# Optimization experiments

Measured on AMD Instinct MI355X. Metric: run time of the kernel, lower is better.

The kernel has to match this reference:

```python
import jax, jax.numpy as jnp
import numpy as np

D_MODEL = 640
KW = 32                                  # kernel_width -> content_kernel (compression (1,1))
SUPER = np.array([5, 5, 2, 1, 1])        # supersampling per subhead
DIL = np.array([1, 1, 2, 4, 8])          # dilation rate per subhead
SUBHEADS = 5
HEADS = int(SUPER.sum())                 # 14
DH = D_MODEL // SUBHEADS                 # 128
B, N = 2, 1024
KC = KW                                  # content kernel width
DIL_PER_HEAD = np.repeat(DIL, SUPER)     # dilation used by each of the 14 value heads


def _windows(seq, bias, dil):
    """Banded (dilated, stride-1, 'same'-padded) windows of a projected sequence.

    seq: (B, N, DH). The original zero-pads the raw sequence, then applies the
    per-head Linear; projecting a zero vector yields the bias, so padding the
    projected sequence with `bias` is mathematically identical.
    Returns (B, N, KC, DH) with out[b, l, j] = padded[b, l + j*dil].
    """
    dil = int(dil)
    pad_total = (KC - 1) * dil           # effective kernel minus 1, stride 1 -> same length
    pl = pad_total // 2
    pr = pad_total - pl
    b = seq.shape[0]
    left = jnp.broadcast_to(bias, (b, pl, DH))
    right = jnp.broadcast_to(bias, (b, pr, DH))
    padded = jnp.concatenate([left, seq, right], axis=1)
    idx = jnp.arange(N)[:, None] + jnp.arange(KC)[None, :] * dil  # (N, KC)
    return padded[:, idx]


def setup_inputs() -> dict:
    key = jax.random.key(0)
    ks = jax.random.split(key, 13)
    f = lambda k, sh, s=1.0: jax.random.normal(k, sh, dtype=jnp.float32) * s
    return {
        "query": f(ks[0], (B, N, D_MODEL)),
        "key": f(ks[1], (B, N, D_MODEL)),
        "value": f(ks[2], (B, N, D_MODEL)),
        "Qk": f(ks[3], (SUBHEADS, DH, D_MODEL), 0.04),
        "Qb": f(ks[4], (SUBHEADS, DH), 0.02),
        "Kk": f(ks[5], (SUBHEADS, DH, D_MODEL), 0.04),
        "Kb": f(ks[6], (SUBHEADS, DH), 0.02),
        "Vk": f(ks[7], (HEADS, DH, D_MODEL), 0.04),
        "Vb": f(ks[8], (HEADS, DH), 0.02),
        "Sk": f(ks[9], (HEADS, KC, KC), 0.1),   # Pos_Sampling kernel, Kq=1 so in=out=KC
        "Sb": f(ks[10], (HEADS, KC), 0.02),
        "Ck": f(ks[11], (D_MODEL, HEADS * DH), 0.02),  # Collapse kernel
        "Cb": f(ks[12], (D_MODEL,), 0.0),
    }


def reference(query, key, value, Qk, Qb, Kk, Kb, Vk, Vb, Sk, Sb, Ck, Cb):
    # Per-subhead Q/K projections (query_kernel=1, stride=1 -> one query per position)
    q = jnp.einsum('bnd,sod->bnso', query, Qk) + Qb          # (B,N,5,DH)
    kproj = jnp.einsum('bnd,sod->bnso', key, Kk) + Kb        # (B,N,5,DH)
    kwin = jnp.stack(
        [_windows(kproj[:, :, s], Kb[s], DIL[s]) for s in range(SUBHEADS)],
        axis=2)                                              # (B,N,5,KC,DH)
    # Banded scores (original applies no 1/sqrt(d) scaling)
    score = jnp.einsum('bnsd,bnskd->bnsk', q, kwin)          # (B,N,5,KC)
    # Supersample subhead scores into heads, then learned positional resampling
    score = jnp.repeat(score, SUPER, axis=2, total_repeat_length=HEADS)  # (B,N,14,KC)
    score = jnp.einsum('bnhk,hjk->bnhj', score, Sk) + Sb     # Pos_Sampling Linear
    w = jax.nn.softmax(score, axis=-1)
    # Per-head value projection; each head windows with its subhead's dilation
    vproj = jnp.einsum('bnd,hod->bnho', value, Vk) + Vb      # (B,N,14,DH)
    vwin = jnp.stack(
        [_windows(vproj[:, :, h], Vb[h], DIL_PER_HEAD[h]) for h in range(HEADS)],
        axis=2)                                              # (B,N,14,KC,DH)
    attn = jnp.einsum('bnhk,bnhkd->bnhd', w, vwin)           # (B,N,14,DH)
    flat = attn.reshape(attn.shape[0], attn.shape[1], HEADS * DH)
    return jnp.einsum('bnf,of->bno', flat, Ck) + Cb          # (B,N,D_MODEL)
```

## Files before the change

### kernel.cpp

```cpp
#include <hip/hip_runtime.h>
#include <hip/hip_bf16.h>

using bf16 = __hip_bfloat16;
typedef __attribute__((ext_vector_type(8))) short s16x8;
typedef __attribute__((ext_vector_type(4))) float f32x4;
typedef unsigned int u32;

__device__ __forceinline__ float b2f(short u) {
    union { float f; u32 i; } x; x.i = ((u32)(unsigned short)u) << 16; return x.f;
}
__device__ __forceinline__ short f2b(float f) {
    bf16 h = (bf16)f; return *(short*)&h;
}

struct CvtArgs { const float* src[10]; bf16* dst[10]; int n[10]; int bb[11]; };
__global__ __launch_bounds__(256)
void convert_kernel(CvtArgs a) {
    const int blk = blockIdx.x;
    int s = 0;
    while (s < 9 && blk >= a.bb[s + 1]) ++s;
    const int base = (blk - a.bb[s]) * 1024 + threadIdx.x * 4;
    if (base >= a.n[s]) return;
    float4 v = *(const float4*)(a.src[s] + base);
    ushort4 o;
    o.x = (unsigned short)f2b(v.x); o.y = (unsigned short)f2b(v.y);
    o.z = (unsigned short)f2b(v.z); o.w = (unsigned short)f2b(v.w);
    *(ushort4*)(a.dst[s] + base) = o;
}

template<int BM, int BN, bool A_F32, bool OUT_F32>
__device__ __forceinline__ void gemm_pipe(
    const void* __restrict__ A, const bf16* __restrict__ W,
    const bf16* __restrict__ bias, void* __restrict__ out,
    int m0, int n0, int N, int K, bf16* lA, bf16* lB) {
    constexpr int WM = BM / 2, WN = BN / 2, FM = WM / 16, FN = WN / 16;
    constexpr int SA = BM / 64, SB = BN / 64;
    const int tid = threadIdx.x;
    const int wave = tid >> 6, lane = tid & 63;
    const int wr = wave >> 1, wc = wave & 1;
    const int quad = lane >> 4, lm = lane & 15;
    uint4 ra[SA], rb[SB];

    auto loadA = [&](int k0) {
#pragma unroll
        for (int q = 0; q < SA; ++q) {
            const int sl = q * 256 + tid, row = sl >> 2, col = (sl & 3) * 8;
            if (A_F32) {
                const float* g = (const float*)A + (size_t)(m0 + row) * K + k0 + col;
                float4 f0 = *(const float4*)g;
                float4 f1 = *(const float4*)(g + 4);
                union { uint4 u; short h[8]; } p;
                p.h[0] = f2b(f0.x); p.h[1] = f2b(f0.y); p.h[2] = f2b(f0.z); p.h[3] = f2b(f0.w);
                p.h[4] = f2b(f1.x); p.h[5] = f2b(f1.y); p.h[6] = f2b(f1.z); p.h[7] = f2b(f1.w);
                ra[q] = p.u;
            } else {
                ra[q] = *(const uint4*)((const bf16*)A + (size_t)(m0 + row) * K + k0 + col);
            }
        }
    };
    auto loadB = [&](int k0) {
#pragma unroll
        for (int q = 0; q < SB; ++q) {
            const int sl = q * 256 + tid, row = sl >> 2, col = (sl & 3) * 8;
            rb[q] = *(const uint4*)(W + (size_t)(n0 + row) * K + k0 + col);
        }
    };

    f32x4 acc[FM][FN] = {};
    loadA(0); loadB(0);
    for (int k0 = 0; k0 < K; k0 += 32) {
#pragma unroll
        for (int q = 0; q < SA; ++q) *(uint4*)(lA + (q * 256 + tid) * 8) = ra[q];
#pragma unroll
        for (int q = 0; q < SB; ++q) *(uint4*)(lB + (q * 256 + tid) * 8) = rb[q];
        __syncthreads();
        if (k0 + 32 < K) { loadA(k0 + 32); loadB(k0 + 32); }
        s16x8 af[FM], bf_[FN];
#pragma unroll
        for (int i = 0; i < FM; ++i)
            af[i] = *(const s16x8*)&lA[(wr * WM + i * 16 + lm) * 32 + quad * 8];
#pragma unroll
        for (int j = 0; j < FN; ++j)
            bf_[j] = *(const s16x8*)&lB[(wc * WN + j * 16 + lm) * 32 + quad * 8];
#pragma unroll
        for (int i = 0; i < FM; ++i)
#pragma unroll
            for (int j = 0; j < FN; ++j)
                acc[i][j] = __builtin_amdgcn_mfma_f32_16x16x32_bf16(af[i], bf_[j], acc[i][j], 0, 0, 0);
        __syncthreads();
    }
#pragma unroll
    for (int i = 0; i < FM; ++i) {
        const int rbase = m0 + wr * WM + i * 16 + quad * 4;
#pragma unroll
        for (int j = 0; j < FN; ++j) {
            const int col = n0 + wc * WN + j * 16 + lm;
            const float bv = (float)bias[col];
#pragma unroll
            for (int r = 0; r < 4; ++r) {
                float v = acc[i][j][r] + bv;
                size_t off = (size_t)(rbase + r) * N + col;
                if (OUT_F32) ((float*)out)[off] = v;
                else         ((bf16*)out)[off] = (bf16)v;
            }
        }
    }
}

__global__ __launch_bounds__(256)
void proj_kernel(const float* __restrict__ q, const float* __restrict__ k,
                 const float* __restrict__ v,
                 const bf16* __restrict__ Qkc, const bf16* __restrict__ Kkc,
                 const bf16* __restrict__ Vkc,
                 const bf16* __restrict__ Qbc, const bf16* __restrict__ Kbc,
                 const bf16* __restrict__ Vbc,
                 float* __restrict__ qp, float* __restrict__ kp,
                 bf16* __restrict__ vp) {
    __shared__ __align__(16) bf16 lA[128 * 32];
    __shared__ __align__(16) bf16 lB[64 * 32];
    const int L = blockIdx.x, xcd = L & 7, i = L >> 3;
    const int m0 = (xcd * 2 + i / 48) * 128;
    const int nid = i % 48;
    if (nid < 10)
        gemm_pipe<128, 64, true, true >(q, Qkc, Qbc, qp, m0, nid * 64, 640, 640, lA, lB);
    else if (nid < 20)
        gemm_pipe<128, 64, true, true >(k, Kkc, Kbc, kp, m0, (nid - 10) * 64, 640, 640, lA, lB);
    else
        gemm_pipe<128, 64, true, false>(v, Vkc, Vbc, vp, m0, (nid - 20) * 64, 1792, 640, lA, lB);
}

__global__ __launch_bounds__(256)
void collapse_kernel(const bf16* __restrict__ atn, const bf16* __restrict__ Ckc,
                     const bf16* __restrict__ Cbc, float* __restrict__ out) {
    __shared__ __align__(16) bf16 lA[64 * 32];
    __shared__ __align__(16) bf16 lB[64 * 32];
    const int L = blockIdx.x, xcd = L & 7, i = L >> 3;
    const int m0 = (xcd * 4 + i / 10) * 64;
    const int n0 = (i % 10) * 64;
    gemm_pipe<64, 64, false, true>(atn, Ckc, Cbc, out, m0, n0, 640, 1792, lA, lB);
}

__global__ __launch_bounds__(256)
void attn_v4(const float* __restrict__ qp, const float* __restrict__ kp,
             const bf16* __restrict__ vp,
             const bf16* __restrict__ Kbc, const bf16* __restrict__ Vbc,
             const bf16* __restrict__ Skc, const bf16* __restrict__ Sbc,
             bf16* __restrict__ atn) {
    const int pos = ((blockIdx.x & 7) << 8) | (blockIdx.x >> 3);
    const int b = pos >> 10, l = pos & 1023;
    const int t = threadIdx.x;
    __shared__ float qs[640];
    __shared__ float sc5[5 * 32];
    __shared__ float sc14[14 * 32];
    __shared__ float w14T[32 * 14];

    if (t < 160) ((float4*)qs)[t] = ((const float4*)(qp + (size_t)pos * 640))[t];
    __syncthreads();

    {
        const int j = t >> 3, p = t & 7;
#pragma unroll
        for (int s = 0; s < 5; ++s) {
            const int dil = (s < 2) ? 1 : (1 << (s - 1));
            const int pl = (31 * dil) >> 1;
            const int row = l + j * dil - pl;
            const float* q = qs + s * 128 + p * 4;
            float acc = 0.f;
            if (row >= 0 && row < 1024) {
                const float* kr = kp + (size_t)((b << 10) | row) * 640 + s * 128 + p * 4;
#pragma unroll
                for (int g = 0; g < 4; ++g) {
                    float4 kv = *(const float4*)(kr + g * 32);
                    float4 qv = *(const float4*)(q + g * 32);
                    acc += qv.x * kv.x + qv.y * kv.y + qv.z * kv.z + qv.w * kv.w;
                }
            } else {
                const bf16* kb = Kbc + s * 128 + p * 4;
#pragma unroll
                for (int g = 0; g < 4; ++g) {
                    float4 qv = *(const float4*)(q + g * 32);
                    acc += qv.x * (float)kb[g * 32] + qv.y * (float)kb[g * 32 + 1]
                         + qv.z * (float)kb[g * 32 + 2] + qv.w * (float)kb[g * 32 + 3];
                }
            }
            acc += __shfl_xor(acc, 1);
            acc += __shfl_xor(acc, 2);
            acc += __shfl_xor(acc, 4);
            if (p == 0) sc5[s * 32 + j] = acc;
        }
    }
    __syncthreads();

    for (int idx = t; idx < 448; idx += 256) {
        const int h = idx >> 5;
        const int s = (h < 5) ? 0 : (h < 10) ? 1 : (h < 12) ? 2 : (h == 12) ? 3 : 4;
        const s16x8* sk = (const s16x8*)((const short*)Skc + idx * 32);
        const float* sc = sc5 + s * 32;
        float acc = b2f(((const short*)Sbc)[idx]);
#pragma unroll
        for (int g = 0; g < 4; ++g) {
            s16x8 kk = sk[g];
#pragma unroll
            for (int r = 0; r < 8; ++r) acc += sc[g * 8 + r] * b2f(kk[r]);
        }
        sc14[idx] = acc;
    }
    __syncthreads();

    if (t < 224) {
        const int h = t >> 4, u = t & 15;
        float s0 = sc14[h * 32 + u], s1 = sc14[h * 32 + u + 16];
        float mx = fmaxf(s0, s1);
#pragma unroll
        for (int m = 1; m < 16; m <<= 1) mx = fmaxf(mx, __shfl_xor(mx, m));
        float e0 = __expf(s0 - mx), e1 = __expf(s1 - mx);
        float sum = e0 + e1;
#pragma unroll
        for (int m = 1; m < 16; m <<= 1) sum += __shfl_xor(sum, m);
        float inv = 1.f / sum;
        w14T[u * 14 + h] = e0 * inv;
        w14T[(u + 16) * 14 + h] = e1 * inv;
    }
    __syncthreads();

    if (t < 224) {
        const int h = t >> 4, d8 = (t & 15) * 8;
        const int dil = (h < 10) ? 1 : (h < 12) ? 2 : (h == 12) ? 4 : 8;
        const int pl = (31 * dil) >> 1;
        const int col = h * 128 + d8;
        float acc[8] = {};
#pragma unroll
        for (int j = 0; j < 32; ++j) {
            const int row = l + j * dil - pl;
            const short* src = (row >= 0 && row < 1024)
                ? (const short*)vp + (size_t)((b << 10) | row) * 1792 + col
                : (const short*)Vbc + col;
            s16x8 v8 = *(const s16x8*)src;
            const float w = w14T[j * 14 + h];
#pragma unroll
            for (int r = 0; r < 8; ++r) acc[r] += w * b2f(v8[r]);
        }
        union { uint4 u; short h16[8]; } o;
#pragma unroll
        for (int r = 0; r < 8; ++r) o.h16[r] = f2b(acc[r]);
        *(uint4*)((short*)atn + (size_t)pos * 1792 + col) = o.u;
    }
}

extern "C" void kernel_launch(void* const* d_in, const int* in_sizes, int n_in,
                              void* d_out, int out_size, void* d_ws, size_t ws_size,
                              hipStream_t stream) {
    const int M = 2048;
    char* w = (char*)d_ws;
    size_t off = 0;
    auto alloc = [&](size_t bytes) -> char* {
        off = (off + 255) & ~(size_t)255;
        char* p = w + off; off += bytes; return p;
    };
    bf16* Qkc = (bf16*)alloc(409600 * 2);
    bf16* Qbc = (bf16*)alloc(640 * 2);
    bf16* Kkc = (bf16*)alloc(409600 * 2);
    bf16* Kbc = (bf16*)alloc(640 * 2);
    bf16* Vkc = (bf16*)alloc(1146880 * 2);
    bf16* Vbc = (bf16*)alloc(1792 * 2);
    bf16* Skc = (bf16*)alloc(14336 * 2);
    bf16* Sbc = (bf16*)alloc(448 * 2);
    bf16* Ckc = (bf16*)alloc(1146880 * 2);
    bf16* Cbc = (bf16*)alloc(640 * 2);
    float* qp = (float*)alloc((size_t)M * 640 * 4);
    float* kp = (float*)alloc((size_t)M * 640 * 4);
    bf16*  vp = (bf16*)alloc((size_t)M * 1792 * 2);
    bf16*  atn = (bf16*)alloc((size_t)M * 1792 * 2);

    CvtArgs ca;
    bf16* dsts[10] = {Qkc, Qbc, Kkc, Kbc, Vkc, Vbc, Skc, Sbc, Ckc, Cbc};
    const int ns[10] = {409600, 640, 409600, 640, 1146880, 1792, 14336, 448, 1146880, 640};
    int cum = 0;
    for (int i = 0; i < 10; ++i) {
        ca.src[i] = (const float*)d_in[3 + i];
        ca.dst[i] = dsts[i];
        ca.n[i] = ns[i];
        ca.bb[i] = cum;
        cum += (ns[i] + 1023) / 1024;
    }
    ca.bb[10] = cum;

    dim3 blk(256);
    convert_kernel<<<dim3(cum), blk, 0, stream>>>(ca);
    proj_kernel<<<dim3(768), blk, 0, stream>>>(
        (const float*)d_in[0], (const float*)d_in[1], (const float*)d_in[2],
        Qkc, Kkc, Vkc, Qbc, Kbc, Vbc, qp, kp, vp);
    attn_v4<<<dim3(2048), blk, 0, stream>>>(qp, kp, vp, Kbc, Vbc, Skc, Sbc, atn);
    collapse_kernel<<<dim3(320), blk, 0, stream>>>(atn, Ckc, Cbc, (float*)d_out);
}
```

Baseline: 165.6 us.

## Process two query positions per attention block and share value-window loads

The attention kernel now handles two positions (l and l+4) per block, launching half as many blocks. Value rows that fall in both positions' dilated windows are loaded once and accumulated into two outputs, with separate thread groups for each dilation class. The aim is to cut redundant global value loads and per-block overhead, at the cost of fewer blocks, lower parallelism and more register use.

```diff
diff --git a/kernel.cpp b/kernel.cpp
--- a/kernel.cpp
+++ b/kernel.cpp
@@ -141,20 +141,25 @@
 }
 
 __global__ __launch_bounds__(256)
-void attn_v4(const float* __restrict__ qp, const float* __restrict__ kp,
+void attn_v5(const float* __restrict__ qp, const float* __restrict__ kp,
              const bf16* __restrict__ vp,
              const bf16* __restrict__ Kbc, const bf16* __restrict__ Vbc,
              const bf16* __restrict__ Skc, const bf16* __restrict__ Sbc,
              bf16* __restrict__ atn) {
-    const int pos = ((blockIdx.x & 7) << 8) | (blockIdx.x >> 3);
-    const int b = pos >> 10, l = pos & 1023;
+    const int blk = blockIdx.x;
+    const int qi = blk >> 3;
+    const int pos0 = ((blk & 7) << 8) + ((qi >> 2) << 3) + (qi & 3);
+    const int b = pos0 >> 10, l0 = pos0 & 1023;
     const int t = threadIdx.x;
-    __shared__ float qs[640];
-    __shared__ float sc5[5 * 32];
-    __shared__ float sc14[14 * 32];
-    __shared__ float w14T[32 * 14];
-
-    if (t < 160) ((float4*)qs)[t] = ((const float4*)(qp + (size_t)pos * 640))[t];
+    __shared__ float qs[2][640];
+    __shared__ float sc5[2][5 * 32];
+    __shared__ float sc14[2][448];
+    __shared__ float w14[2][32][14];
+
+    for (int i = t; i < 320; i += 256) {
+        const int pp = i / 160, c = i % 160;
+        ((float4*)qs[pp])[c] = ((const float4*)(qp + (size_t)(pos0 + 4 * pp) * 640))[c];
+    }
     __syncthreads();
 
     {
@@ -163,39 +168,43 @@
         for (int s = 0; s < 5; ++s) {
             const int dil = (s < 2) ? 1 : (1 << (s - 1));
             const int pl = (31 * dil) >> 1;
-            const int row = l + j * dil - pl;
-            const float* q = qs + s * 128 + p * 4;
-            float acc = 0.f;
-            if (row >= 0 && row < 1024) {
-                const float* kr = kp + (size_t)((b << 10) | row) * 640 + s * 128 + p * 4;
-#pragma unroll
-                for (int g = 0; g < 4; ++g) {
-                    float4 kv = *(const float4*)(kr + g * 32);
-                    float4 qv = *(const float4*)(q + g * 32);
-                    acc += qv.x * kv.x + qv.y * kv.y + qv.z * kv.z + qv.w * kv.w;
+#pragma unroll
+            for (int pp = 0; pp < 2; ++pp) {
+                const int row = l0 + 4 * pp + j * dil - pl;
+                const float* qv = qs[pp] + s * 128 + p * 4;
+                float acc = 0.f;
+                if (row >= 0 && row < 1024) {
+                    const float* kr = kp + (size_t)((b << 10) | row) * 640 + s * 128 + p * 4;
+#pragma unroll
+                    for (int g = 0; g < 4; ++g) {
+                        float4 kv = *(const float4*)(kr + g * 32);
+                        float4 qq = *(const float4*)(qv + g * 32);
+                        acc += qq.x * kv.x + qq.y * kv.y + qq.z * kv.z + qq.w * kv.w;
+                    }
+                } else {
+                    const bf16* kb = Kbc + s * 128 + p * 4;
+#pragma unroll
+                    for (int g = 0; g < 4; ++g) {
+                        float4 qq = *(const float4*)(qv + g * 32);
+                        acc += qq.x * (float)kb[g * 32] + qq.y * (float)kb[g * 32 + 1]
+                             + qq.z * (float)kb[g * 32 + 2] + qq.w * (float)kb[g * 32 + 3];
+                    }
                 }
-            } else {
-                const bf16* kb = Kbc + s * 128 + p * 4;
-#pragma unroll
-                for (int g = 0; g < 4; ++g) {
-                    float4 qv = *(const float4*)(q + g * 32);
-                    acc += qv.x * (float)kb[g * 32] + qv.y * (float)kb[g * 32 + 1]
-                         + qv.z * (float)kb[g * 32 + 2] + qv.w * (float)kb[g * 32 + 3];
-                }
-            }
-            acc += __shfl_xor(acc, 1);
-            acc += __shfl_xor(acc, 2);
-            acc += __shfl_xor(acc, 4);
-            if (p == 0) sc5[s * 32 + j] = acc;
+                acc += __shfl_xor(acc, 1);
+                acc += __shfl_xor(acc, 2);
+                acc += __shfl_xor(acc, 4);
+                if (p == 0) sc5[pp][s * 32 + j] = acc;
+            }
         }
     }
     __syncthreads();
 
-    for (int idx = t; idx < 448; idx += 256) {
+    for (int ii = t; ii < 896; ii += 256) {
+        const int pp = ii / 448, idx = ii % 448;
         const int h = idx >> 5;
         const int s = (h < 5) ? 0 : (h < 10) ? 1 : (h < 12) ? 2 : (h == 12) ? 3 : 4;
         const s16x8* sk = (const s16x8*)((const short*)Skc + idx * 32);
-        const float* sc = sc5 + s * 32;
+        const float* sc = sc5[pp] + s * 32;
         float acc = b2f(((const short*)Sbc)[idx]);
 #pragma unroll
         for (int g = 0; g < 4; ++g) {
@@ -203,47 +212,132 @@
 #pragma unroll
             for (int r = 0; r < 8; ++r) acc += sc[g * 8 + r] * b2f(kk[r]);
         }
-        sc14[idx] = acc;
+        sc14[pp][idx] = acc;
     }
     __syncthreads();
 
     if (t < 224) {
         const int h = t >> 4, u = t & 15;
-        float s0 = sc14[h * 32 + u], s1 = sc14[h * 32 + u + 16];
-        float mx = fmaxf(s0, s1);
-#pragma unroll
-        for (int m = 1; m < 16; m <<= 1) mx = fmaxf(mx, __shfl_xor(mx, m));
-        float e0 = __expf(s0 - mx), e1 = __expf(s1 - mx);
-        float sum = e0 + e1;
-#pragma unroll
-        for (int m = 1; m < 16; m <<= 1) sum += __shfl_xor(sum, m);
-        float inv = 1.f / sum;
-        w14T[u * 14 + h] = e0 * inv;
-        w14T[(u + 16) * 14 + h] = e1 * inv;
+#pragma unroll
+        for (int pp = 0; pp < 2; ++pp) {
+            float s0 = sc14[pp][h * 32 + u], s1 = sc14[pp][h * 32 + u + 16];
+            float mx = fmaxf(s0, s1);
+#pragma unroll
+            for (int m = 1; m < 16; m <<= 1) mx = fmaxf(mx, __shfl_xor(mx, m));
+            float e0 = __expf(s0 - mx), e1 = __expf(s1 - mx);
+            float sum = e0 + e1;
+#pragma unroll
+            for (int m = 1; m < 16; m <<= 1) sum += __shfl_xor(sum, m);
+            float inv = 1.f / sum;
+            w14[pp][u][h] = e0 * inv;
+            w14[pp][u + 16][h] = e1 * inv;
+        }
     }
     __syncthreads();
 
-    if (t < 224) {
-        const int h = t >> 4, d8 = (t & 15) * 8;
-        const int dil = (h < 10) ? 1 : (h < 12) ? 2 : (h == 12) ? 4 : 8;
-        const int pl = (31 * dil) >> 1;
-        const int col = h * 128 + d8;
-        float acc[8] = {};
-#pragma unroll
-        for (int j = 0; j < 32; ++j) {
-            const int row = l + j * dil - pl;
+    const size_t vbase = (size_t)b << 10;
+    if (t < 160) {
+        const int h = t >> 4, d8 = (t & 15) * 8, col = h * 128 + d8;
+        float acc[2][8] = {};
+        for (int rr = 0; rr < 36; ++rr) {
+            const int row = l0 - 15 + rr;
             const short* src = (row >= 0 && row < 1024)
-                ? (const short*)vp + (size_t)((b << 10) | row) * 1792 + col
+                ? (const short*)vp + (vbase | (size_t)row) * 1792 + col
                 : (const short*)Vbc + col;
             s16x8 v8 = *(const s16x8*)src;
-            const float w = w14T[j * 14 + h];
+            const int j0 = rr, j1 = rr - 4;
+            if (j0 < 32) {
+                const float w = w14[0][j0][h];
+#pragma unroll
+                for (int r = 0; r < 8; ++r) acc[0][r] += w * b2f(v8[r]);
+            }
+            if (j1 >= 0) {
+                const float w = w14[1][j1][h];
+#pragma unroll
+                for (int r = 0; r < 8; ++r) acc[1][r] += w * b2f(v8[r]);
+            }
+        }
+#pragma unroll
+        for (int pp = 0; pp < 2; ++pp) {
+            union { uint4 u; short h16[8]; } o;
+#pragma unroll
+            for (int r = 0; r < 8; ++r) o.h16[r] = f2b(acc[pp][r]);
+            *(uint4*)((short*)atn + (size_t)(pos0 + 4 * pp) * 1792 + col) = o.u;
+        }
+    } else if (t < 192) {
+        const int idx = t - 160, h = 10 + (idx >> 4), d8 = (idx & 15) * 8, col = h * 128 + d8;
+        float acc[2][8] = {};
+        for (int rr = 0; rr < 34; ++rr) {
+            const int row = l0 - 31 + 2 * rr;
+            const short* src = (row >= 0 && row < 1024)
+                ? (const short*)vp + (vbase | (size_t)row) * 1792 + col
+                : (const short*)Vbc + col;
+            s16x8 v8 = *(const s16x8*)src;
+            const int j0 = rr, j1 = rr - 2;
+            if (j0 < 32) {
+                const float w = w14[0][j0][h];
+#pragma unroll
+                for (int r = 0; r < 8; ++r) acc[0][r] += w * b2f(v8[r]);
+            }
+            if (j1 >= 0 && j1 < 32) {
+                const float w = w14[1][j1][h];
+#pragma unroll
+                for (int r = 0; r < 8; ++r) acc[1][r] += w * b2f(v8[r]);
+            }
+        }
+#pragma unroll
+        for (int pp = 0; pp < 2; ++pp) {
+            union { uint4 u; short h16[8]; } o;
+#pragma unroll
+            for (int r = 0; r < 8; ++r) o.h16[r] = f2b(acc[pp][r]);
+            *(uint4*)((short*)atn + (size_t)(pos0 + 4 * pp) * 1792 + col) = o.u;
+        }
+    } else if (t < 208) {
+        const int d8 = (t - 192) * 8, col = 12 * 128 + d8;
+        float acc[2][8] = {};
+        for (int rr = 0; rr < 33; ++rr) {
+            const int row = l0 - 62 + 4 * rr;
+            const short* src = (row >= 0 && row < 1024)
+                ? (const short*)vp + (vbase | (size_t)row) * 1792 + col
+                : (const short*)Vbc + col;
+            s16x8 v8 = *(const s16x8*)src;
+            const int j0 = rr, j1 = rr - 1;
+            if (j0 < 32) {
+                const float w = w14[0][j0][12];
+#pragma unroll
+                for (int r = 0; r < 8; ++r) acc[0][r] += w * b2f(v8[r]);
+            }
+            if (j1 >= 0 && j1 < 32) {
+                const float w = w14[1][j1][12];
+#pragma unroll
+                for (int r = 0; r < 8; ++r) acc[1][r] += w * b2f(v8[r]);
+            }
+        }
+#pragma unroll
+        for (int pp = 0; pp < 2; ++pp) {
+            union { uint4 u; short h16[8]; } o;
+#pragma unroll
+            for (int r = 0; r < 8; ++r) o.h16[r] = f2b(acc[pp][r]);
+            *(uint4*)((short*)atn + (size_t)(pos0 + 4 * pp) * 1792 + col) = o.u;
+        }
+    } else if (t < 240) {
+        const int idx = t - 208, pp = idx & 1, d8 = (idx >> 1) * 8, col = 13 * 128 + d8;
+        const int l = l0 + 4 * pp;
+        float acc[8] = {};
+        for (int j = 0; j < 32; ++j) {
+            const int row = l + 8 * j - 124;
+            const short* src = (row >= 0 && row < 1024)
+                ? (const short*)vp + (vbase | (size_t)row) * 1792 + col
+                : (const short*)Vbc + col;
+            s16x8 v8 = *(const s16x8*)src;
+            const float w = w14[pp][j][13];
 #pragma unroll
             for (int r = 0; r < 8; ++r) acc[r] += w * b2f(v8[r]);
         }
         union { uint4 u; short h16[8]; } o;
 #pragma unroll
         for (int r = 0; r < 8; ++r) o.h16[r] = f2b(acc[r]);
-        *(uint4*)((short*)atn + (size_t)pos * 1792 + col) = o.u;
+        *(uint4*)((short*)atn + (size_t)(pos0 + 4 * pp) * 1792 + col) = o.u;
     }
 }
 
@@ -290,6 +384,6 @@
     proj_kernel<<<dim3(768), blk, 0, stream>>>(
         (const float*)d_in[0], (const float*)d_in[1], (const float*)d_in[2],
         Qkc, Kkc, Vkc, Qbc, Kbc, Vbc, qp, kp, vp);
-    attn_v4<<<dim3(2048), blk, 0, stream>>>(qp, kp, vp, Kbc, Vbc, Skc, Sbc, atn);
+    attn_v5<<<dim3(1024), blk, 0, stream>>>(qp, kp, vp, Kbc, Vbc, Skc, Sbc, atn);
     collapse_kernel<<<dim3(320), blk, 0, stream>>>(atn, Ckc, Cbc, (float*)d_out);
 }
```

Result: no change. 168.8 us (+1.9%).
